# Kernel tuning notes

Measured on AMD Instinct MI355X. Metric: run time of the kernel, lower is better.

Reference implementation:

```python
import jax, jax.numpy as jnp
import numpy as np

B, S, D = 2, 2048, 2048
H, DH = 16, 128          # n_heads, head_dim
HFF = 8192               # hidden_dim (SwiGLU)
EPS = 1e-5               # layer_norm_eps passed to AdvancedRMSNorm


def setup_inputs() -> dict:
    key = jax.random.key(0)
    ks = jax.random.split(key, 16)
    sd = lambda fan_in: 1.0 / np.sqrt(fan_in)
    inp = {
        "x": jax.random.normal(ks[0], (B, S, D), jnp.float32),
        # attention (torch Linear weights: [out, in])
        "q_w": jax.random.normal(ks[1], (D, D), jnp.float32) * sd(D),
        "k_w": jax.random.normal(ks[2], (D, D), jnp.float32) * sd(D),
        "v_w": jax.random.normal(ks[3], (D, D), jnp.float32) * sd(D),
        "o_w": jax.random.normal(ks[4], (D, D), jnp.float32) * sd(D),
        "temp": jnp.ones((H, 1, 1), jnp.float32),  # learnable per-head temperature
        # RMSNorm scales
        "ln1_w": jnp.ones((D,), jnp.float32),
        "ln2_w": jnp.ones((D,), jnp.float32),
        # SwiGLU
        "gate_w": jax.random.normal(ks[5], (HFF, D), jnp.float32) * sd(D),
        "up_w": jax.random.normal(ks[6], (HFF, D), jnp.float32) * sd(D),
        "gate2_w": jax.random.normal(ks[7], (HFF, D), jnp.float32) * sd(D),
        "down_w": jax.random.normal(ks[8], (D, HFF), jnp.float32) * sd(HFF),
        # gated residual connections (Linear with bias)
        "ag_w": jax.random.normal(ks[9], (D, D), jnp.float32) * sd(D),
        "ag_b": jnp.zeros((D,), jnp.float32),
        "fg_w": jax.random.normal(ks[10], (D, D), jnp.float32) * sd(D),
        "fg_b": jnp.zeros((D,), jnp.float32),
    }
    return inp


def _rmsnorm(x, w):
    rms = jnp.sqrt(jnp.mean(x * x, axis=-1, keepdims=True) + EPS)
    return w * (x / rms)


def _l2norm(x):
    # F.normalize(dim=-1): x / max(||x||_2, 1e-12)
    n = jnp.sqrt(jnp.sum(x * x, axis=-1, keepdims=True))
    return x / jnp.maximum(n, 1e-12)


def _block(x, q_w, k_w, v_w, o_w, temp, ln1_w, ln2_w,
           gate_w, up_w, gate2_w, down_w, ag_w, ag_b, fg_w, fg_b):
    # --- cosine-sim attention sublayer ---
    residual = x
    h = _rmsnorm(x, ln1_w)
    q = (h @ q_w.T).reshape(B, S, H, DH).transpose(0, 2, 1, 3)  # [B,H,S,DH]
    k = (h @ k_w.T).reshape(B, S, H, DH).transpose(0, 2, 1, 3)
    v = (h @ v_w.T).reshape(B, S, H, DH).transpose(0, 2, 1, 3)
    q = _l2norm(q)
    k = _l2norm(k)
    scores = jnp.einsum("bhqd,bhkd->bhqk", q, k) * temp  # temp [H,1,1] broadcasts
    causal = jnp.triu(jnp.ones((S, S), bool), k=1)
    scores = jnp.where(causal, -jnp.inf, scores)
    attn = jax.nn.softmax(scores, axis=-1)
    out = jnp.einsum("bhqk,bhkd->bhqd", attn, v)
    out = out.transpose(0, 2, 1, 3).reshape(B, S, D)
    attn_out = out @ o_w.T
    # gated residual: sigmoid(W a + b)*a + (1-g)*residual
    g = jax.nn.sigmoid(attn_out @ ag_w.T + ag_b)
    x = g * attn_out + (1.0 - g) * residual
    # --- SwiGLU sublayer ---
    residual = x
    h = _rmsnorm(x, ln2_w)
    gate = jax.nn.silu(h @ gate_w.T)
    up = h @ up_w.T
    gate2 = jax.nn.sigmoid(h @ gate2_w.T)
    ffn_out = (gate * up * gate2) @ down_w.T
    g = jax.nn.sigmoid(ffn_out @ fg_w.T + fg_b)
    return g * ffn_out + (1.0 - g) * residual


def reference(x, q_w, k_w, v_w, o_w, temp, ln1_w, ln2_w,
              gate_w, up_w, gate2_w, down_w, ag_w, ag_b, fg_w, fg_b):
    return _block(x, q_w, k_w, v_w, o_w, temp, ln1_w, ln2_w,
                  gate_w, up_w, gate2_w, down_w, ag_w, ag_b, fg_w, fg_b)
```

## Files before the change

### kernel.cpp

```cpp
#include <hip/hip_runtime.h>

typedef unsigned short u16;
typedef unsigned int u32;
using bf16x8 = __attribute__((ext_vector_type(8))) short;
using f32x4  = __attribute__((ext_vector_type(4))) float;

#define EPS 1e-5f

__device__ __forceinline__ u16 f2bf(float f) {
    union { float f; u32 u; } v; v.f = f;
    u32 r = v.u + 0x7FFFu + ((v.u >> 16) & 1u);
    return (u16)(r >> 16);
}
__device__ __forceinline__ float bf2f(u16 u) {
    union { u32 u; float f; } v; v.u = ((u32)u) << 16;
    return v.f;
}
__device__ __forceinline__ void gl16(const void* g, void* s) {
    __builtin_amdgcn_global_load_lds(
        (const __attribute__((address_space(1))) u32*)g,
        (__attribute__((address_space(3))) u32*)s, 16, 0, 0);
}
__device__ __forceinline__ float sigm(float x) { return 1.f / (1.f + __expf(-x)); }

__global__ void conv_bf16(const float* __restrict__ src, u16* __restrict__ dst, int n4) {
    int i = blockIdx.x * 256 + threadIdx.x;
    if (i >= n4) return;
    float4 v = reinterpret_cast<const float4*>(src)[i];
    u32 lo = (u32)f2bf(v.x) | ((u32)f2bf(v.y) << 16);
    u32 hi = (u32)f2bf(v.z) | ((u32)f2bf(v.w) << 16);
    reinterpret_cast<uint2*>(dst)[i] = make_uint2(lo, hi);
}

__global__ void conv3_bf16(const float* __restrict__ s0, const float* __restrict__ s1,
                           const float* __restrict__ s2, u16* __restrict__ d0,
                           u16* __restrict__ d1, u16* __restrict__ d2, int n4) {
    int i = blockIdx.x * 256 + threadIdx.x;
    if (i >= n4) return;
    const float* src = (blockIdx.y == 0) ? s0 : (blockIdx.y == 1) ? s1 : s2;
    u16* dst = (blockIdx.y == 0) ? d0 : (blockIdx.y == 1) ? d1 : d2;
    float4 v = reinterpret_cast<const float4*>(src)[i];
    u32 lo = (u32)f2bf(v.x) | ((u32)f2bf(v.y) << 16);
    u32 hi = (u32)f2bf(v.z) | ((u32)f2bf(v.w) << 16);
    reinterpret_cast<uint2*>(dst)[i] = make_uint2(lo, hi);
}

__global__ void rmsnorm_k(const float* __restrict__ x, const float* __restrict__ wt,
                          u16* __restrict__ out) {
    __shared__ float red[4];
    const int row = blockIdx.x, t = threadIdx.x;
    const float* xr = x + (size_t)row * 2048;
    float4 v0 = *reinterpret_cast<const float4*>(&xr[t * 8]);
    float4 v1 = *reinterpret_cast<const float4*>(&xr[t * 8 + 4]);
    float ss = v0.x*v0.x + v0.y*v0.y + v0.z*v0.z + v0.w*v0.w
             + v1.x*v1.x + v1.y*v1.y + v1.z*v1.z + v1.w*v1.w;
#pragma unroll
    for (int d = 1; d < 64; d <<= 1) ss += __shfl_xor(ss, d);
    if ((t & 63) == 0) red[t >> 6] = ss;
    __syncthreads();
    const float tot = red[0] + red[1] + red[2] + red[3];
    const float s = 1.f / sqrtf(tot * (1.f / 2048.f) + EPS);
    float4 w0 = *reinterpret_cast<const float4*>(&wt[t * 8]);
    float4 w1 = *reinterpret_cast<const float4*>(&wt[t * 8 + 4]);
    u32 o[4];
    o[0] = (u32)f2bf(v0.x * s * w0.x) | ((u32)f2bf(v0.y * s * w0.y) << 16);
    o[1] = (u32)f2bf(v0.z * s * w0.z) | ((u32)f2bf(v0.w * s * w0.w) << 16);
    o[2] = (u32)f2bf(v1.x * s * w1.x) | ((u32)f2bf(v1.y * s * w1.y) << 16);
    o[3] = (u32)f2bf(v1.z * s * w1.z) | ((u32)f2bf(v1.w * s * w1.w) << 16);
    *reinterpret_cast<uint4*>(&out[(size_t)row * 2048 + t * 8]) =
        make_uint4(o[0], o[1], o[2], o[3]);
}

__global__ void qk_l2norm(u16* __restrict__ qkv, const float* __restrict__ temp) {
    const int wid = blockIdx.x * 4 + (threadIdx.x >> 6);
    const int l = threadIdx.x & 63;
    const int n = wid >> 5;
    const int rem = wid & 31;
    const int which = rem >> 4;
    const int h = rem & 15;
    u16* p = qkv + (size_t)n * 6144 + which * 2048 + h * 128 + l * 2;
    u32 v = *reinterpret_cast<const u32*>(p);
    float f0 = bf2f((u16)(v & 0xffff)), f1 = bf2f((u16)(v >> 16));
    float ss = f0 * f0 + f1 * f1;
#pragma unroll
    for (int d = 1; d < 64; d <<= 1) ss += __shfl_xor(ss, d);
    float sc = 1.f / fmaxf(sqrtf(ss), 1e-12f);
    if (which == 0) sc *= temp[h];
    *reinterpret_cast<u32*>(p) = (u32)f2bf(f0 * sc) | ((u32)f2bf(f1 * sc) << 16);
}

template <int EPI>
__global__ __launch_bounds__(512, 1)
void gemm_bt(const u16* __restrict__ A, const u16* __restrict__ B,
             float* __restrict__ outF, u16* __restrict__ outB,
             const float* __restrict__ bias, const float* __restrict__ addend,
             const float* __restrict__ resid, float* __restrict__ outG,
             int M, int N, int K, int ldc) {
    extern __shared__ u16 lds[];
    const int nbn = N >> 8;
    const int nwg = (M >> 7) * nbn;
    const int orig = blockIdx.x;
    const int q8 = nwg >> 3, r8 = nwg & 7;
    const int xcd = orig & 7, lin = orig >> 3;
    const int wgid = (xcd < r8 ? xcd * (q8 + 1) : r8 * (q8 + 1) + (xcd - r8) * q8) + lin;
    const int g = wgid / (nbn << 3);
    const int rem = wgid - g * (nbn << 3);
    const int bn = rem >> 3;
    const int bm = (g << 3) + (rem & 7);

    const int t = threadIdx.x;
    const int w = t >> 6, l = t & 63;
    const int wr = w >> 2, wc = w & 3;
    const int lr = l & 15, lg = l >> 4;
    const int NT = K >> 6;

    const int pr = t >> 3, ps = t & 7;
    const int sg = ps ^ (pr & 7);
    const u16* aSrc = A + (size_t)(bm * 128 + pr) * K + sg * 8;
    const u16* bSrc = B + (size_t)(bn * 256 + pr) * K + sg * 8;
    const size_t rowStep = (size_t)64 * K;

#define STAGE_P0(TT, bi) do {                                                   \
        u16* da = lds + (bi) * 24576 + t * 8;                                   \
        gl16(aSrc + (size_t)(TT) * 64, da);                                     \
        gl16(aSrc + rowStep + (size_t)(TT) * 64, da + 4096);                    \
        gl16(bSrc + (size_t)(TT) * 64, lds + (bi) * 24576 + 8192 + t * 8);      \
    } while (0)
#define STAGE_P1(TT, bi) do {                                                   \
        u16* db = lds + (bi) * 24576 + 8192 + t * 8;                            \
        gl16(bSrc + rowStep + (size_t)(TT) * 64, db + 4096);                    \
        gl16(bSrc + 2 * rowStep + (size_t)(TT) * 64, db + 8192);                \
        gl16(bSrc + 3 * rowStep + (size_t)(TT) * 64, db + 12288);               \
    } while (0)

    f32x4 acc[4][4];
#pragma unroll
    for (int i = 0; i < 4; i++)
#pragma unroll
        for (int j = 0; j < 4; j++) acc[i][j] = (f32x4){0.f, 0.f, 0.f, 0.f};

    const int xr = (lr & 7) << 4;
    const int kof0 = ((lg) << 4) ^ xr;
    const int kof1 = ((4 + lg) << 4) ^ xr;

    STAGE_P0(0, 0); STAGE_P1(0, 0);
    if (NT > 1) {
        STAGE_P0(1, 1); STAGE_P1(1, 1);
        asm volatile("s_waitcnt vmcnt(6)" ::: "memory");
    } else {
        asm volatile("s_waitcnt vmcnt(0)" ::: "memory");
    }
    __builtin_amdgcn_s_barrier();

    for (int T = 0; T < NT; ++T) {
        const int bi = T % 3;
        const int sbi = (T + 2) % 3;
        const bool st = (T + 2) < NT;
        const char* bufA = (const char*)(lds + bi * 24576);
        const char* bufB = bufA + 16384;
        bf16x8 bf[4][2], af[2][2];
#pragma unroll
        for (int n = 0; n < 4; n++) {
            const int rb = wc * 64 + n * 16 + lr;
            bf[n][0] = *reinterpret_cast<const bf16x8*>(bufB + rb * 128 + kof0);
            bf[n][1] = *reinterpret_cast<const bf16x8*>(bufB + rb * 128 + kof1);
        }
#pragma unroll
        for (int m = 0; m < 2; m++) {
            const int ra = wr * 64 + m * 16 + lr;
            af[m][0] = *reinterpret_cast<const bf16x8*>(bufA + ra * 128 + kof0);
            af[m][1] = *reinterpret_cast<const bf16x8*>(bufA + ra * 128 + kof1);
        }
        if (st) STAGE_P0(T + 2, sbi);
        __builtin_amdgcn_s_barrier();
        __builtin_amdgcn_s_setprio(1);
#pragma unroll
        for (int m = 0; m < 2; m++)
#pragma unroll
            for (int n = 0; n < 4; n++) {
                acc[m][n] = __builtin_amdgcn_mfma_f32_16x16x32_bf16(af[m][0], bf[n][0], acc[m][n], 0, 0, 0);
                acc[m][n] = __builtin_amdgcn_mfma_f32_16x16x32_bf16(af[m][1], bf[n][1], acc[m][n], 0, 0, 0);
            }
        __builtin_amdgcn_s_setprio(0);
        __builtin_amdgcn_s_barrier();
        bf16x8 ag[2][2];
#pragma unroll
        for (int m = 0; m < 2; m++) {
            const int ra = wr * 64 + (m + 2) * 16 + lr;
            ag[m][0] = *reinterpret_cast<const bf16x8*>(bufA + ra * 128 + kof0);
            ag[m][1] = *reinterpret_cast<const bf16x8*>(bufA + ra * 128 + kof1);
        }
        if (st) STAGE_P1(T + 2, sbi);
        __builtin_amdgcn_s_barrier();
        __builtin_amdgcn_s_setprio(1);
#pragma unroll
        for (int m = 0; m < 2; m++)
#pragma unroll
            for (int n = 0; n < 4; n++) {
                acc[m + 2][n] = __builtin_amdgcn_mfma_f32_16x16x32_bf16(ag[m][0], bf[n][0], acc[m + 2][n], 0, 0, 0);
                acc[m + 2][n] = __builtin_amdgcn_mfma_f32_16x16x32_bf16(ag[m][1], bf[n][1], acc[m + 2][n], 0, 0, 0);
            }
        __builtin_amdgcn_s_setprio(0);
        if (st) {
            asm volatile("s_waitcnt vmcnt(6)" ::: "memory");
        } else if (T + 1 < NT) {
            asm volatile("s_waitcnt vmcnt(0)" ::: "memory");
        }
        __builtin_amdgcn_s_barrier();
    }
#undef STAGE_P0
#undef STAGE_P1

#pragma unroll
    for (int m = 0; m < 4; m++) {
        const int row = bm * 128 + wr * 64 + m * 16 + lg * 4;
#pragma unroll
        for (int n = 0; n < 4; n++) {
            const int col = bn * 256 + wc * 64 + n * 16 + lr;
#pragma unroll
            for (int q = 0; q < 4; q++) {
                const size_t idx = (size_t)(row + q) * ldc + col;
                const float v = acc[m][n][q];
                if (EPI == 0) {
                    outB[idx] = f2bf(v);
                } else if (EPI == 1) {
                    outF[idx] = v;
                    outB[idx] = f2bf(v);
                } else {
                    const float g2 = sigm(v + bias[col]);
                    outG[idx] = g2 * addend[idx] + (1.f - g2) * resid[idx];
                }
            }
        }
    }
}

#define VSWZ(dh) (((((dh) >> 3) ^ (dh)) & 7) << 4)
__global__ __launch_bounds__(512) void flash_attn(const u16* __restrict__ qkv,
                                                  u16* __restrict__ out) {
    __shared__ u16 klds[2][64 * 128];
    __shared__ u16 vlds[2][128 * 64];
    __shared__ u16 plds[8][16 * 64];
    const int t = threadIdx.x, w = t >> 6, l = t & 63;
    const int lr = l & 15, lg = l >> 4;
    const int b0 = blockIdx.x;
    const int xcd = b0 & 7, i0 = b0 >> 3;
    const int bh = ((i0 & 3) << 3) | xcd;
    const int p = i0 >> 2;
    const int b = bh >> 4, h = bh & 15;
    const size_t base = (size_t)b * 2048;
    const int sr0 = t >> 4;
    const int sc0 = (t & 15) << 3;

    uint4 kreg0, kreg1, vreg0, vreg1;

#define STAGE_LOAD(KT) do {                                                          \
        const size_t gg = (base + (size_t)(KT) * 64 + sr0) * 6144 + h * 128 + sc0;   \
        kreg0 = *reinterpret_cast<const uint4*>(&qkv[gg + 2048]);                    \
        vreg0 = *reinterpret_cast<const uint4*>(&qkv[gg + 4096]);                    \
        kreg1 = *reinterpret_cast<const uint4*>(&qkv[gg + 32 * 6144 + 2048]);        \
        vreg1 = *reinterpret_cast<const uint4*>(&qkv[gg + 32 * 6144 + 4096]);        \
    } while (0)

#define STAGE_WRITE(BUF) do {                                                                     \
        char* kb = (char*)&klds[BUF][0];                                                          \
        char* vb = (char*)&vlds[BUF][0];                                                          \
        *reinterpret_cast<uint4*>(kb + ((sr0 * 256 + sc0 * 2) ^ ((sr0 & 7) << 4))) = kreg0;       \
        *reinterpret_cast<uint4*>(kb + (((sr0 + 32) * 256 + sc0 * 2) ^ ((sr0 & 7) << 4))) = kreg1;\
        union { uint4 u; u16 s[8]; } vv;                                                          \
        vv.u = vreg0;                                                                             \
        _Pragma("unroll")                                                                         \
        for (int jj = 0; jj < 8; jj++) {                                                          \
            const int dh = sc0 + jj;                                                              \
            *reinterpret_cast<u16*>(vb + ((dh * 128 + sr0 * 2) ^ VSWZ(dh))) = vv.s[jj];           \
        }                                                                                         \
        vv.u = vreg1;                                                                             \
        _Pragma("unroll")                                                                         \
        for (int jj = 0; jj < 8; jj++) {                                                          \
            const int dh = sc0 + jj;                                                              \
            *reinterpret_cast<u16*>(vb + ((dh * 128 + (sr0 + 32) * 2) ^ VSWZ(dh))) = vv.s[jj];    \
        }                                                                                         \
    } while (0)

    for (int phase = 0; phase < 2; ++phase) {
        const int qt = phase ? (15 - p) : p;
        const int last = 2 * qt + 1;
        const int qrow = qt * 128 + w * 16 + lr;
        const int qr0 = qt * 128 + w * 16 + lg * 4;
        bf16x8 qf[4];
#pragma unroll
        for (int kk = 0; kk < 4; kk++)
            qf[kk] = *reinterpret_cast<const bf16x8*>(
                &qkv[(base + qrow) * 6144 + h * 128 + kk * 32 + lg * 8]);
        f32x4 o[8];
#pragma unroll
        for (int i = 0; i < 8; i++) o[i] = (f32x4){0.f, 0.f, 0.f, 0.f};
        float m[4] = {-1e30f, -1e30f, -1e30f, -1e30f};
        float ls[4] = {0.f, 0.f, 0.f, 0.f};

        STAGE_LOAD(0);
        int cur = 0;
        STAGE_WRITE(0);
        __syncthreads();

        for (int kt = 0; kt <= last; ++kt) {
            if (kt < last) STAGE_LOAD(kt + 1);
            const char* kb = (const char*)&klds[cur][0];
            const char* vb = (const char*)&vlds[cur][0];
            f32x4 s[4];
#pragma unroll
            for (int nf = 0; nf < 4; nf++) {
                f32x4 a = (f32x4){0.f, 0.f, 0.f, 0.f};
                const int kv = nf * 16 + lr;
#pragma unroll
                for (int kk = 0; kk < 4; kk++) {
                    bf16x8 kf = *reinterpret_cast<const bf16x8*>(
                        kb + ((kv * 256 + kk * 64 + lg * 16) ^ ((kv & 7) << 4)));
                    a = __builtin_amdgcn_mfma_f32_16x16x32_bf16(qf[kk], kf, a, 0, 0, 0);
                }
                s[nf] = a;
            }
            if (kt >= 2 * qt) {
#pragma unroll
                for (int nf = 0; nf < 4; nf++) {
                    const int kvi = kt * 64 + nf * 16 + lr;
#pragma unroll
                    for (int q = 0; q < 4; q++)
                        if (kvi > qr0 + q) s[nf][q] = -1e30f;
                }
            }
            float mx[4] = {-1e30f, -1e30f, -1e30f, -1e30f};
#pragma unroll
            for (int nf = 0; nf < 4; nf++)
#pragma unroll
                for (int q = 0; q < 4; q++) mx[q] = fmaxf(mx[q], s[nf][q]);
#pragma unroll
            for (int q = 0; q < 4; q++) {
#pragma unroll
                for (int d = 1; d < 16; d <<= 1) mx[q] = fmaxf(mx[q], __shfl_xor(mx[q], d));
            }
            float fac[4], rs[4];
#pragma unroll
            for (int q = 0; q < 4; q++) {
                const float mn = fmaxf(m[q], mx[q]);
                fac[q] = __expf(m[q] - mn);
                m[q] = mn;
                rs[q] = 0.f;
            }
#pragma unroll
            for (int nf = 0; nf < 4; nf++) {
#pragma unroll
                for (int q = 0; q < 4; q++) {
                    const float pv = __expf(s[nf][q] - m[q]);
                    s[nf][q] = pv;
                    rs[q] += pv;
                }
            }
#pragma unroll
            for (int nf = 0; nf < 4; nf++) {
                const int col = nf * 16 + lr;
#pragma unroll
                for (int q = 0; q < 4; q++) {
                    const int row = lg * 4 + q;
                    *reinterpret_cast<u16*>((char*)&plds[w][0] +
                        ((row * 128 + col * 2) ^ ((row & 7) << 4))) = f2bf(s[nf][q]);
                }
            }
#pragma unroll
            for (int q = 0; q < 4; q++) {
#pragma unroll
                for (int d = 1; d < 16; d <<= 1) rs[q] += __shfl_xor(rs[q], d);
                ls[q] = ls[q] * fac[q] + rs[q];
            }
#pragma unroll
            for (int nf2 = 0; nf2 < 8; nf2++)
#pragma unroll
                for (int q = 0; q < 4; q++) o[nf2][q] *= fac[q];
#pragma unroll
            for (int ks = 0; ks < 2; ks++) {
                bf16x8 pf = *reinterpret_cast<const bf16x8*>((char*)&plds[w][0] +
                    ((lr * 128 + ks * 64 + lg * 16) ^ ((lr & 7) << 4)));
#pragma unroll
                for (int nf2 = 0; nf2 < 8; nf2++) {
                    const int dh = nf2 * 16 + lr;
                    bf16x8 vf = *reinterpret_cast<const bf16x8*>(
                        vb + ((dh * 128 + ks * 64 + lg * 16) ^ VSWZ(dh)));
                    o[nf2] = __builtin_amdgcn_mfma_f32_16x16x32_bf16(pf, vf, o[nf2], 0, 0, 0);
                }
            }
            if (kt < last) STAGE_WRITE(cur ^ 1);
            __syncthreads();
            cur ^= 1;
        }
#pragma unroll
        for (int nf2 = 0; nf2 < 8; nf2++) {
            const int col = h * 128 + nf2 * 16 + lr;
#pragma unroll
            for (int q = 0; q < 4; q++) {
                const float v = o[nf2][q] / ls[q];
                out[(base + qr0 + q) * 2048 + col] = f2bf(v);
            }
        }
        __syncthreads();
    }
#undef STAGE_LOAD
#undef STAGE_WRITE
}

__global__ void swiglu_comb(const u16* __restrict__ f3, u16* __restrict__ comb) {
    const size_t u = (size_t)blockIdx.x * 256 + threadIdx.x;
    const size_t n = u >> 8;
    const int f = (int)(u & 255) << 3;
    const u16* gp = f3 + n * 6144 + f;
    union { uint4 q; u16 s[8]; } g, up, g2;
    g.q  = *reinterpret_cast<const uint4*>(gp);
    up.q = *reinterpret_cast<const uint4*>(gp + 2048);
    g2.q = *reinterpret_cast<const uint4*>(gp + 4096);
    u32 r[4];
#pragma unroll
    for (int i = 0; i < 4; i++) {
        float a0 = bf2f(g.s[2 * i]),     a1 = bf2f(g.s[2 * i + 1]);
        float b0 = bf2f(up.s[2 * i]),    b1 = bf2f(up.s[2 * i + 1]);
        float c0 = bf2f(g2.s[2 * i]),    c1 = bf2f(g2.s[2 * i + 1]);
        float r0 = a0 * sigm(a0) * b0 * sigm(c0);
        float r1 = a1 * sigm(a1) * b1 * sigm(c1);
        r[i] = (u32)f2bf(r0) | ((u32)f2bf(r1) << 16);
    }
    *reinterpret_cast<uint4*>(comb + n * 8192 + f) = make_uint4(r[0], r[1], r[2], r[3]);
}

extern "C" void kernel_launch(void* const* d_in, const int* in_sizes, int n_in,
                              void* d_out, int out_size, void* d_ws, size_t ws_size,
                              hipStream_t stream) {
    const float* x      = (const float*)d_in[0];
    const float* q_w    = (const float*)d_in[1];
    const float* k_w    = (const float*)d_in[2];
    const float* v_w    = (const float*)d_in[3];
    const float* o_w    = (const float*)d_in[4];
    const float* temp   = (const float*)d_in[5];
    const float* ln1_w  = (const float*)d_in[6];
    const float* ln2_w  = (const float*)d_in[7];
    const float* gate_w = (const float*)d_in[8];
    const float* up_w   = (const float*)d_in[9];
    const float* gate2_w= (const float*)d_in[10];
    const float* down_w = (const float*)d_in[11];
    const float* ag_w   = (const float*)d_in[12];
    const float* ag_b   = (const float*)d_in[13];
    const float* fg_w   = (const float*)d_in[14];
    const float* fg_b   = (const float*)d_in[15];

    const int GEMM_LDS = 147456;
    (void)hipFuncSetAttribute(reinterpret_cast<const void*>(&gemm_bt<0>),
                              hipFuncAttributeMaxDynamicSharedMemorySize, GEMM_LDS);
    (void)hipFuncSetAttribute(reinterpret_cast<const void*>(&gemm_bt<1>),
                              hipFuncAttributeMaxDynamicSharedMemorySize, GEMM_LDS);
    (void)hipFuncSetAttribute(reinterpret_cast<const void*>(&gemm_bt<2>),
                              hipFuncAttributeMaxDynamicSharedMemorySize, GEMM_LDS);

    char* ws = (char*)d_ws;
    u16*  Wbuf = (u16*)(ws);
    u16*  hbuf = (u16*)(ws + 33554432);
    float* x1  = (float*)(ws + 50331648);
    u16*  combo= (u16*)(ws + 83886080);
    char* E    = ws + 150994944;
    char* F    = ws + 201326592;
    u16*  ffb  = (u16*)(ws + 234881024);

    u16*   qkvact = (u16*)E;
    float* aof    = (float*)E;
    u16*   aob    = (u16*)(E + 33554432);
    u16*   ffn3q  = (u16*)E;
    u16*   attnb  = (u16*)F;
    float* fff    = (float*)F;

    float* outp = (float*)d_out;
    const size_t DD = 2048ull * 2048ull;
    const int cg_d = (int)(DD / 4) / 256;
    const int GRID_BIG = 32 * 24;
    const int GRID_SM  = 32 * 8;

    hipLaunchKernelGGL(rmsnorm_k, dim3(4096), dim3(256), 0, stream, x, ln1_w, hbuf);

    hipLaunchKernelGGL(conv3_bf16, dim3(cg_d, 3), dim3(256), 0, stream,
                       q_w, k_w, v_w, Wbuf, Wbuf + DD, Wbuf + 2 * DD, (int)(DD / 4));
    hipLaunchKernelGGL((gemm_bt<0>), dim3(GRID_BIG), dim3(512), GEMM_LDS, stream,
                       hbuf, Wbuf, (float*)nullptr, qkvact,
                       (const float*)nullptr, (const float*)nullptr, (const float*)nullptr,
                       (float*)nullptr, 4096, 6144, 2048, 6144);

    hipLaunchKernelGGL(qk_l2norm, dim3(32768), dim3(256), 0, stream, qkvact, temp);

    hipLaunchKernelGGL(flash_attn, dim3(256), dim3(512), 0, stream, qkvact, attnb);

    hipLaunchKernelGGL(conv_bf16, dim3(cg_d), dim3(256), 0, stream, o_w, Wbuf, (int)(DD / 4));
    hipLaunchKernelGGL((gemm_bt<1>), dim3(GRID_SM), dim3(512), GEMM_LDS, stream,
                       attnb, Wbuf, aof, aob,
                       (const float*)nullptr, (const float*)nullptr, (const float*)nullptr,
                       (float*)nullptr, 4096, 2048, 2048, 2048);

    hipLaunchKernelGGL(conv_bf16, dim3(cg_d), dim3(256), 0, stream, ag_w, Wbuf, (int)(DD / 4));
    hipLaunchKernelGGL((gemm_bt<2>), dim3(GRID_SM), dim3(512), GEMM_LDS, stream,
                       aob, Wbuf, (float*)nullptr, (u16*)nullptr,
                       ag_b, aof, x, x1, 4096, 2048, 2048, 2048);

    hipLaunchKernelGGL(rmsnorm_k, dim3(4096), dim3(256), 0, stream, x1, ln2_w, hbuf);

    for (int qd = 0; qd < 4; qd++) {
        const size_t wofs = (size_t)qd * 2048 * 2048;
        hipLaunchKernelGGL(conv3_bf16, dim3(cg_d, 3), dim3(256), 0, stream,
                           gate_w + wofs, up_w + wofs, gate2_w + wofs,
                           Wbuf, Wbuf + 2048 * 2048, Wbuf + 2ull * 2048 * 2048, (int)(DD / 4));
        hipLaunchKernelGGL((gemm_bt<0>), dim3(GRID_BIG), dim3(512), GEMM_LDS, stream,
                           hbuf, Wbuf, (float*)nullptr, ffn3q,
                           (const float*)nullptr, (const float*)nullptr, (const float*)nullptr,
                           (float*)nullptr, 4096, 6144, 2048, 6144);
        hipLaunchKernelGGL(swiglu_comb, dim3(4096), dim3(256), 0, stream, ffn3q, combo + qd * 2048);
    }

    hipLaunchKernelGGL(conv_bf16, dim3(16384), dim3(256), 0, stream, down_w, Wbuf, (int)(2048ull * 8192 / 4));
    hipLaunchKernelGGL((gemm_bt<1>), dim3(GRID_SM), dim3(512), GEMM_LDS, stream,
                       combo, Wbuf, fff, ffb,
                       (const float*)nullptr, (const float*)nullptr, (const float*)nullptr,
                       (float*)nullptr, 4096, 2048, 8192, 2048);

    hipLaunchKernelGGL(conv_bf16, dim3(cg_d), dim3(256), 0, stream, fg_w, Wbuf, (int)(DD / 4));
    hipLaunchKernelGGL((gemm_bt<2>), dim3(GRID_SM), dim3(512), GEMM_LDS, stream,
                       ffb, Wbuf, (float*)nullptr, (u16*)nullptr,
                       fg_b, fff, x1, outp, 4096, 2048, 2048, 2048);
}
```

Measured before the change: 1.134 ms.

## Add 256x256-tile bf16 GEMM kernel for the wide QKV and FFN projections

Adds a dedicated gemm_big kernel that computes 256x256 output tiles per workgroup instead of 128x256. It double-buffers 64-wide K slices in LDS with async global-to-LDS loads, uses an XOR-swizzled layout, and raises wave priority around the MFMA blocks. It replaces the generic gemm_bt<0> for the 4096x6144x2048 QKV and the four gate/up/gate2 GEMMs, halving the grid to 384 workgroups. The larger tile raises arithmetic intensity and cuts redundant operand loads. In exchange it uses more accumulator registers per thread, and the smaller grid fills the CUs less evenly.

New measurement: 1.186 ms. 4.6% more time.

```diff
diff --git a/kernel.cpp b/kernel.cpp
--- a/kernel.cpp
+++ b/kernel.cpp
@@ -87,6 +87,119 @@
     float sc = 1.f / fmaxf(sqrtf(ss), 1e-12f);
     if (which == 0) sc *= temp[h];
     *reinterpret_cast<u32*>(p) = (u32)f2bf(f0 * sc) | ((u32)f2bf(f1 * sc) << 16);
+}
+
+__global__ __launch_bounds__(512, 1)
+void gemm_big(const u16* __restrict__ A, const u16* __restrict__ B,
+              u16* __restrict__ outB, int M, int N, int K, int ldc) {
+    extern __shared__ u16 lds[];
+    const int nbn = N >> 8;
+    const int nwg = (M >> 8) * nbn;
+    const int orig = blockIdx.x;
+    const int q8 = nwg >> 3, r8 = nwg & 7;
+    const int xcd = orig & 7, lin = orig >> 3;
+    const int wgid = (xcd < r8 ? xcd * (q8 + 1) : r8 * (q8 + 1) + (xcd - r8) * q8) + lin;
+    const int g = wgid / (nbn << 2);
+    const int rem = wgid - g * (nbn << 2);
+    const int bn = rem >> 2;
+    const int bm = (g << 2) + (rem & 3);
+
+    const int t = threadIdx.x;
+    const int w = t >> 6, l = t & 63;
+    const int lr = l & 15, lg = l >> 4;
+    const int NT = K >> 6;
+
+    const int srow = t >> 3;
+    const int scg  = (t & 7) ^ (srow & 7);
+    const u16* aS0 = A + (size_t)(bm * 256 + srow) * K + scg * 8;
+    const u16* aS1 = aS0 + (size_t)128 * K;
+    const u16* bS0 = B + (size_t)(bn * 256 + srow) * K + scg * 8;
+    const u16* bS1 = bS0 + (size_t)128 * K;
+    const size_t r64 = (size_t)64 * K;
+
+#define STG(slot, src, ko) do {                                     \
+        gl16((src) + (ko), (slot) + t * 8);                         \
+        gl16((src) + (ko) + r64, (slot) + 4096 + t * 8);            \
+    } while (0)
+
+    f32x4 acc[16][2];
+#pragma unroll
+    for (int i = 0; i < 16; i++) { acc[i][0] = (f32x4){0,0,0,0}; acc[i][1] = (f32x4){0,0,0,0}; }
+
+    const int xr = (lr & 7) << 4;
+    const int kof[2] = { ((lg) << 4) ^ xr, ((4 + lg) << 4) ^ xr };
+
+    STG(lds + 16384, bS0, 0);
+    STG(lds + 24576, bS1, 0);
+    STG(lds + 0,     aS0, 0);
+    STG(lds + 8192,  aS1, 0);
+    asm volatile("s_waitcnt vmcnt(2)" ::: "memory");
+    __builtin_amdgcn_s_barrier();
+
+    for (int T = 0; T < NT; ++T) {
+        const char* rb = (const char*)lds + (size_t)(T & 1) * 65536;
+        u16* sb = lds + ((T + 1) & 1) * 32768;
+        const bool st = (T + 1) < NT;
+        const size_t ko = (size_t)(T + 1) * 64;
+        bf16x8 bfr[2][2];
+#pragma unroll
+        for (int p = 0; p < 4; ++p) {
+            bf16x8 af[4][2];
+#pragma unroll
+            for (int m2 = 0; m2 < 4; m2++) {
+                const int hrow = (p & 1) * 64 + m2 * 16 + lr;
+                const char* ab = rb + (p >> 1) * 16384 + hrow * 128;
+                af[m2][0] = *reinterpret_cast<const bf16x8*>(ab + kof[0]);
+                af[m2][1] = *reinterpret_cast<const bf16x8*>(ab + kof[1]);
+            }
+            if (p == 0) {
+#pragma unroll
+                for (int n = 0; n < 2; n++) {
+                    const int hrow = (w & 3) * 32 + n * 16 + lr;
+                    const char* bb = rb + 32768 + (w >> 2) * 16384 + hrow * 128;
+                    bfr[n][0] = *reinterpret_cast<const bf16x8*>(bb + kof[0]);
+                    bfr[n][1] = *reinterpret_cast<const bf16x8*>(bb + kof[1]);
+                }
+            }
+            if (st) {
+                if (p == 0) STG(sb + 16384, bS0, ko);
+                if (p == 1) STG(sb + 24576, bS1, ko);
+                if (p == 2) STG(sb + 0,     aS0, ko);
+                if (p == 3) STG(sb + 8192,  aS1, ko);
+            }
+            __builtin_amdgcn_s_barrier();
+            __builtin_amdgcn_s_setprio(1);
+#pragma unroll
+            for (int m2 = 0; m2 < 4; m2++)
+#pragma unroll
+                for (int n = 0; n < 2; n++) {
+                    acc[p * 4 + m2][n] = __builtin_amdgcn_mfma_f32_16x16x32_bf16(
+                        af[m2][0], bfr[n][0], acc[p * 4 + m2][n], 0, 0, 0);
+                    acc[p * 4 + m2][n] = __builtin_amdgcn_mfma_f32_16x16x32_bf16(
+                        af[m2][1], bfr[n][1], acc[p * 4 + m2][n], 0, 0, 0);
+                }
+            __builtin_amdgcn_s_setprio(0);
+            if (p == 1) {
+                if (st) asm volatile("s_waitcnt vmcnt(4)" ::: "memory");
+                else    asm volatile("s_waitcnt vmcnt(0)" ::: "memory");
+            }
+            if (p == 3 && st) asm volatile("s_waitcnt vmcnt(2)" ::: "memory");
+            __builtin_amdgcn_s_barrier();
+        }
+    }
+#undef STG
+
+#pragma unroll
+    for (int m = 0; m < 16; m++) {
+        const int row = bm * 256 + m * 16 + lg * 4;
+#pragma unroll
+        for (int n = 0; n < 2; n++) {
+            const int col = bn * 256 + w * 32 + n * 16 + lr;
+#pragma unroll
+            for (int q = 0; q < 4; q++)
+                outB[(size_t)(row + q) * ldc + col] = f2bf(acc[m][n][q]);
+        }
+    }
 }
 
 template <int EPI>
@@ -450,12 +563,15 @@
     const float* fg_b   = (const float*)d_in[15];
 
     const int GEMM_LDS = 147456;
+    const int BIG_LDS  = 131072;
     (void)hipFuncSetAttribute(reinterpret_cast<const void*>(&gemm_bt<0>),
                               hipFuncAttributeMaxDynamicSharedMemorySize, GEMM_LDS);
     (void)hipFuncSetAttribute(reinterpret_cast<const void*>(&gemm_bt<1>),
                               hipFuncAttributeMaxDynamicSharedMemorySize, GEMM_LDS);
     (void)hipFuncSetAttribute(reinterpret_cast<const void*>(&gemm_bt<2>),
                               hipFuncAttributeMaxDynamicSharedMemorySize, GEMM_LDS);
+    (void)hipFuncSetAttribute(reinterpret_cast<const void*>(&gemm_big),
+                              hipFuncAttributeMaxDynamicSharedMemorySize, BIG_LDS);
 
     char* ws = (char*)d_ws;
     u16*  Wbuf = (u16*)(ws);
@@ -476,17 +592,15 @@
     float* outp = (float*)d_out;
     const size_t DD = 2048ull * 2048ull;
     const int cg_d = (int)(DD / 4) / 256;
-    const int GRID_BIG = 32 * 24;
+    const int GRID_BIG = 16 * 24;
     const int GRID_SM  = 32 * 8;
 
     hipLaunchKernelGGL(rmsnorm_k, dim3(4096), dim3(256), 0, stream, x, ln1_w, hbuf);
 
     hipLaunchKernelGGL(conv3_bf16, dim3(cg_d, 3), dim3(256), 0, stream,
                        q_w, k_w, v_w, Wbuf, Wbuf + DD, Wbuf + 2 * DD, (int)(DD / 4));
-    hipLaunchKernelGGL((gemm_bt<0>), dim3(GRID_BIG), dim3(512), GEMM_LDS, stream,
-                       hbuf, Wbuf, (float*)nullptr, qkvact,
-                       (const float*)nullptr, (const float*)nullptr, (const float*)nullptr,
-                       (float*)nullptr, 4096, 6144, 2048, 6144);
+    hipLaunchKernelGGL(gemm_big, dim3(GRID_BIG), dim3(512), BIG_LDS, stream,
+                       hbuf, Wbuf, qkvact, 4096, 6144, 2048, 6144);
 
     hipLaunchKernelGGL(qk_l2norm, dim3(32768), dim3(256), 0, stream, qkvact, temp);
 
@@ -510,10 +624,8 @@
         hipLaunchKernelGGL(conv3_bf16, dim3(cg_d, 3), dim3(256), 0, stream,
                            gate_w + wofs, up_w + wofs, gate2_w + wofs,
                            Wbuf, Wbuf + 2048 * 2048, Wbuf + 2ull * 2048 * 2048, (int)(DD / 4));
-        hipLaunchKernelGGL((gemm_bt<0>), dim3(GRID_BIG), dim3(512), GEMM_LDS, stream,
-                           hbuf, Wbuf, (float*)nullptr, ffn3q,
-                           (const float*)nullptr, (const float*)nullptr, (const float*)nullptr,
-                           (float*)nullptr, 4096, 6144, 2048, 6144);
+        hipLaunchKernelGGL(gemm_big, dim3(GRID_BIG), dim3(512), BIG_LDS, stream,
+                           hbuf, Wbuf, ffn3q, 4096, 6144, 2048, 6144);
         hipLaunchKernelGGL(swiglu_comb, dim3(4096), dim3(256), 0, stream, ffn3q, combo + qd * 2048);
     }
 
```

## Restructure GEMM mainloop to double-buffered LDS with staggered loads across MFMA phases

Applied to the files above, without the earlier changes.

Replaces the triple-buffered LDS pipeline, which has two barriers per half-step, with a double-buffered scheme. The A and B tile loads for the next K step are spread over four MFMA phases, and there is one wait plus one barrier per iteration. LDS use falls from 144KB to 96KB. In exchange there is less prefetch depth, since loads are one stage ahead instead of two, and a full vmcnt(0) wait each iteration, so memory latency may be exposed more.

After: 1.098 ms. 1.03x faster.

```diff
diff --git a/kernel.cpp b/kernel.cpp
--- a/kernel.cpp
+++ b/kernel.cpp
@@ -91,11 +91,11 @@
 
 template <int EPI>
 __global__ __launch_bounds__(512, 1)
-void gemm_bt(const u16* __restrict__ A, const u16* __restrict__ B,
-             float* __restrict__ outF, u16* __restrict__ outB,
-             const float* __restrict__ bias, const float* __restrict__ addend,
-             const float* __restrict__ resid, float* __restrict__ outG,
-             int M, int N, int K, int ldc) {
+void gemm_u(const u16* __restrict__ A, const u16* __restrict__ B,
+            float* __restrict__ outF, u16* __restrict__ outB,
+            const float* __restrict__ bias, const float* __restrict__ addend,
+            const float* __restrict__ resid, float* __restrict__ outG,
+            int M, int N, int K, int ldc) {
     extern __shared__ u16 lds[];
     const int nbn = N >> 8;
     const int nwg = (M >> 7) * nbn;
@@ -120,18 +120,13 @@
     const u16* bSrc = B + (size_t)(bn * 256 + pr) * K + sg * 8;
     const size_t rowStep = (size_t)64 * K;
 
-#define STAGE_P0(TT, bi) do {                                                   \
-        u16* da = lds + (bi) * 24576 + t * 8;                                   \
-        gl16(aSrc + (size_t)(TT) * 64, da);                                     \
-        gl16(aSrc + rowStep + (size_t)(TT) * 64, da + 4096);                    \
-        gl16(bSrc + (size_t)(TT) * 64, lds + (bi) * 24576 + 8192 + t * 8);      \
-    } while (0)
-#define STAGE_P1(TT, bi) do {                                                   \
-        u16* db = lds + (bi) * 24576 + 8192 + t * 8;                            \
-        gl16(bSrc + rowStep + (size_t)(TT) * 64, db + 4096);                    \
-        gl16(bSrc + 2 * rowStep + (size_t)(TT) * 64, db + 8192);                \
-        gl16(bSrc + 3 * rowStep + (size_t)(TT) * 64, db + 12288);               \
-    } while (0)
+#define STG_A(bi, ko) do { u16* da = lds + (bi) * 24576 + t * 8;                 \
+        gl16(aSrc + (ko), da); gl16(aSrc + rowStep + (ko), da + 4096); } while (0)
+#define STG_B01(bi, ko) do { u16* db = lds + (bi) * 24576 + 8192 + t * 8;        \
+        gl16(bSrc + (ko), db); gl16(bSrc + rowStep + (ko), db + 4096); } while (0)
+#define STG_B23(bi, ko) do { u16* db = lds + (bi) * 24576 + 8192 + t * 8;        \
+        gl16(bSrc + 2 * rowStep + (ko), db + 8192);                              \
+        gl16(bSrc + 3 * rowStep + (ko), db + 12288); } while (0)
 
     f32x4 acc[4][4];
 #pragma unroll
@@ -140,76 +135,56 @@
         for (int j = 0; j < 4; j++) acc[i][j] = (f32x4){0.f, 0.f, 0.f, 0.f};
 
     const int xr = (lr & 7) << 4;
-    const int kof0 = ((lg) << 4) ^ xr;
-    const int kof1 = ((4 + lg) << 4) ^ xr;
-
-    STAGE_P0(0, 0); STAGE_P1(0, 0);
-    if (NT > 1) {
-        STAGE_P0(1, 1); STAGE_P1(1, 1);
-        asm volatile("s_waitcnt vmcnt(6)" ::: "memory");
-    } else {
-        asm volatile("s_waitcnt vmcnt(0)" ::: "memory");
-    }
+    const int kof[2] = { ((lg) << 4) ^ xr, ((4 + lg) << 4) ^ xr };
+
+    STG_A(0, 0); STG_B01(0, 0); STG_B23(0, 0);
+    asm volatile("s_waitcnt vmcnt(0)" ::: "memory");
     __builtin_amdgcn_s_barrier();
 
     for (int T = 0; T < NT; ++T) {
-        const int bi = T % 3;
-        const int sbi = (T + 2) % 3;
-        const bool st = (T + 2) < NT;
-        const char* bufA = (const char*)(lds + bi * 24576);
+        const char* bufA = (const char*)lds + (size_t)(T & 1) * 49152;
         const char* bufB = bufA + 16384;
-        bf16x8 bf[4][2], af[2][2];
+        const int sbi = (T + 1) & 1;
+        const bool st = (T + 1) < NT;
+        const size_t ko = (size_t)(T + 1) * 64;
+        bf16x8 bf[4][2];
 #pragma unroll
         for (int n = 0; n < 4; n++) {
             const int rb = wc * 64 + n * 16 + lr;
-            bf[n][0] = *reinterpret_cast<const bf16x8*>(bufB + rb * 128 + kof0);
-            bf[n][1] = *reinterpret_cast<const bf16x8*>(bufB + rb * 128 + kof1);
+            bf[n][0] = *reinterpret_cast<const bf16x8*>(bufB + rb * 128 + kof[0]);
+            bf[n][1] = *reinterpret_cast<const bf16x8*>(bufB + rb * 128 + kof[1]);
         }
 #pragma unroll
-        for (int m = 0; m < 2; m++) {
-            const int ra = wr * 64 + m * 16 + lr;
-            af[m][0] = *reinterpret_cast<const bf16x8*>(bufA + ra * 128 + kof0);
-            af[m][1] = *reinterpret_cast<const bf16x8*>(bufA + ra * 128 + kof1);
+        for (int p = 0; p < 4; ++p) {
+            const int ks = p >> 1, mh = p & 1;
+            bf16x8 af[2];
+#pragma unroll
+            for (int m2 = 0; m2 < 2; m2++) {
+                const int ra = wr * 64 + (mh * 2 + m2) * 16 + lr;
+                af[m2] = *reinterpret_cast<const bf16x8*>(bufA + ra * 128 + kof[ks]);
+            }
+            if (st) {
+                if (p == 0) STG_A(sbi, ko);
+                if (p == 1) STG_B01(sbi, ko);
+                if (p == 2) STG_B23(sbi, ko);
+            }
+            __builtin_amdgcn_s_setprio(1);
+#pragma unroll
+            for (int m2 = 0; m2 < 2; m2++)
+#pragma unroll
+                for (int n = 0; n < 4; n++)
+                    acc[mh * 2 + m2][n] = __builtin_amdgcn_mfma_f32_16x16x32_bf16(
+                        af[m2], bf[n][ks], acc[mh * 2 + m2][n], 0, 0, 0);
+            __builtin_amdgcn_s_setprio(0);
         }
-        if (st) STAGE_P0(T + 2, sbi);
-        __builtin_amdgcn_s_barrier();
-        __builtin_amdgcn_s_setprio(1);
-#pragma unroll
-        for (int m = 0; m < 2; m++)
-#pragma unroll
-            for (int n = 0; n < 4; n++) {
-                acc[m][n] = __builtin_amdgcn_mfma_f32_16x16x32_bf16(af[m][0], bf[n][0], acc[m][n], 0, 0, 0);
-                acc[m][n] = __builtin_amdgcn_mfma_f32_16x16x32_bf16(af[m][1], bf[n][1], acc[m][n], 0, 0, 0);
-            }
-        __builtin_amdgcn_s_setprio(0);
-        __builtin_amdgcn_s_barrier();
-        bf16x8 ag[2][2];
-#pragma unroll
-        for (int m = 0; m < 2; m++) {
-            const int ra = wr * 64 + (m + 2) * 16 + lr;
-            ag[m][0] = *reinterpret_cast<const bf16x8*>(bufA + ra * 128 + kof0);
-            ag[m][1] = *reinterpret_cast<const bf16x8*>(bufA + ra * 128 + kof1);
+        if (st) {
+            asm volatile("s_waitcnt vmcnt(0)" ::: "memory");
+            __builtin_amdgcn_s_barrier();
         }
-        if (st) STAGE_P1(T + 2, sbi);
-        __builtin_amdgcn_s_barrier();
-        __builtin_amdgcn_s_setprio(1);
-#pragma unroll
-        for (int m = 0; m < 2; m++)
-#pragma unroll
-            for (int n = 0; n < 4; n++) {
-                acc[m + 2][n] = __builtin_amdgcn_mfma_f32_16x16x32_bf16(ag[m][0], bf[n][0], acc[m + 2][n], 0, 0, 0);
-                acc[m + 2][n] = __builtin_amdgcn_mfma_f32_16x16x32_bf16(ag[m][1], bf[n][1], acc[m + 2][n], 0, 0, 0);
-            }
-        __builtin_amdgcn_s_setprio(0);
-        if (st) {
-            asm volatile("s_waitcnt vmcnt(6)" ::: "memory");
-        } else if (T + 1 < NT) {
-            asm volatile("s_waitcnt vmcnt(0)" ::: "memory");
-        }
-        __builtin_amdgcn_s_barrier();
     }
-#undef STAGE_P0
-#undef STAGE_P1
+#undef STG_A
+#undef STG_B01
+#undef STG_B23
 
 #pragma unroll
     for (int m = 0; m < 4; m++) {
@@ -449,12 +424,12 @@
     const float* fg_w   = (const float*)d_in[14];
     const float* fg_b   = (const float*)d_in[15];
 
-    const int GEMM_LDS = 147456;
-    (void)hipFuncSetAttribute(reinterpret_cast<const void*>(&gemm_bt<0>),
+    const int GEMM_LDS = 98304;
+    (void)hipFuncSetAttribute(reinterpret_cast<const void*>(&gemm_u<0>),
                               hipFuncAttributeMaxDynamicSharedMemorySize, GEMM_LDS);
-    (void)hipFuncSetAttribute(reinterpret_cast<const void*>(&gemm_bt<1>),
+    (void)hipFuncSetAttribute(reinterpret_cast<const void*>(&gemm_u<1>),
                               hipFuncAttributeMaxDynamicSharedMemorySize, GEMM_LDS);
-    (void)hipFuncSetAttribute(reinterpret_cast<const void*>(&gemm_bt<2>),
+    (void)hipFuncSetAttribute(reinterpret_cast<const void*>(&gemm_u<2>),
                               hipFuncAttributeMaxDynamicSharedMemorySize, GEMM_LDS);
 
     char* ws = (char*)d_ws;
@@ -483,7 +458,7 @@
 
     hipLaunchKernelGGL(conv3_bf16, dim3(cg_d, 3), dim3(256), 0, stream,
                        q_w, k_w, v_w, Wbuf, Wbuf + DD, Wbuf + 2 * DD, (int)(DD / 4));
-    hipLaunchKernelGGL((gemm_bt<0>), dim3(GRID_BIG), dim3(512), GEMM_LDS, stream,
+    hipLaunchKernelGGL((gemm_u<0>), dim3(GRID_BIG), dim3(512), GEMM_LDS, stream,
                        hbuf, Wbuf, (float*)nullptr, qkvact,
                        (const float*)nullptr, (const float*)nullptr, (const float*)nullptr,
                        (float*)nullptr, 4096, 6144, 2048, 6144);
@@ -493,13 +468,13 @@
     hipLaunchKernelGGL(flash_attn, dim3(256), dim3(512), 0, stream, qkvact, attnb);
 
     hipLaunchKernelGGL(conv_bf16, dim3(cg_d), dim3(256), 0, stream, o_w, Wbuf, (int)(DD / 4));
-    hipLaunchKernelGGL((gemm_bt<1>), dim3(GRID_SM), dim3(512), GEMM_LDS, stream,
+    hipLaunchKernelGGL((gemm_u<1>), dim3(GRID_SM), dim3(512), GEMM_LDS, stream,
                        attnb, Wbuf, aof, aob,
                        (const float*)nullptr, (const float*)nullptr, (const float*)nullptr,
                        (float*)nullptr, 4096, 2048, 2048, 2048);
 
     hipLaunchKernelGGL(conv_bf16, dim3(cg_d), dim3(256), 0, stream, ag_w, Wbuf, (int)(DD / 4));
-    hipLaunchKernelGGL((gemm_bt<2>), dim3(GRID_SM), dim3(512), GEMM_LDS, stream,
+    hipLaunchKernelGGL((gemm_u<2>), dim3(GRID_SM), dim3(512), GEMM_LDS, stream,
                        aob, Wbuf, (float*)nullptr, (u16*)nullptr,
                        ag_b, aof, x, x1, 4096, 2048, 2048, 2048);
 
@@ -510,7 +485,7 @@
         hipLaunchKernelGGL(conv3_bf16, dim3(cg_d, 3), dim3(256), 0, stream,
                            gate_w + wofs, up_w + wofs, gate2_w + wofs,
                            Wbuf, Wbuf + 2048 * 2048, Wbuf + 2ull * 2048 * 2048, (int)(DD / 4));
-        hipLaunchKernelGGL((gemm_bt<0>), dim3(GRID_BIG), dim3(512), GEMM_LDS, stream,
+        hipLaunchKernelGGL((gemm_u<0>), dim3(GRID_BIG), dim3(512), GEMM_LDS, stream,
                            hbuf, Wbuf, (float*)nullptr, ffn3q,
                            (const float*)nullptr, (const float*)nullptr, (const float*)nullptr,
                            (float*)nullptr, 4096, 6144, 2048, 6144);
@@ -518,13 +493,13 @@
     }
 
     hipLaunchKernelGGL(conv_bf16, dim3(16384), dim3(256), 0, stream, down_w, Wbuf, (int)(2048ull * 8192 / 4));
-    hipLaunchKernelGGL((gemm_bt<1>), dim3(GRID_SM), dim3(512), GEMM_LDS, stream,
+    hipLaunchKernelGGL((gemm_u<1>), dim3(GRID_SM), dim3(512), GEMM_LDS, stream,
                        combo, Wbuf, fff, ffb,
                        (const float*)nullptr, (const float*)nullptr, (const float*)nullptr,
                        (float*)nullptr, 4096, 2048, 8192, 2048);
 
     hipLaunchKernelGGL(conv_bf16, dim3(cg_d), dim3(256), 0, stream, fg_w, Wbuf, (int)(DD / 4));
-    hipLaunchKernelGGL((gemm_bt<2>), dim3(GRID_SM), dim3(512), GEMM_LDS, stream,
+    hipLaunchKernelGGL((gemm_u<2>), dim3(GRID_SM), dim3(512), GEMM_LDS, stream,
                        ffb, Wbuf, (float*)nullptr, (u16*)nullptr,
                        fg_b, fff, x1, outp, 4096, 2048, 2048, 2048);
 }
```
